# Performance work log

Measured on AMD Instinct MI355X. Metric: run time of the kernel, lower is better.

The kernel has to match this reference:

```python
import jax, jax.numpy as jnp
import numpy as np


def setup_inputs() -> dict:
    key = jax.random.key(0)
    k1, k2 = jax.random.split(key)
    B, N, D = 32, 2048, 3
    x = jax.random.normal(k1, (B, N, D), dtype=jnp.float32)
    y = jax.random.normal(k2, (B, N, D), dtype=jnp.float32)
    return {"x": x, "y": y}


def reference(x, y):
    # Batched squared euclidean distance matrix [B, N, M] without
    # materializing the [B, N, M, D] difference tensor.
    x2 = jnp.sum(x * x, axis=-1)                      # [B, N]
    y2 = jnp.sum(y * y, axis=-1)                      # [B, M]
    xy = jnp.einsum('bnd,bmd->bnm', x, y)             # [B, N, M]
    dist = x2[:, :, None] + y2[:, None, :] - 2.0 * xy # squared cdist
    dist = jnp.maximum(dist, 0.0)
    in_dist_out = jnp.min(dist, axis=1)               # min over N -> [B, M]
    out_dist_in = jnp.min(dist, axis=2)               # min over M -> [B, N]
    num_pts = x.shape[0]                              # batch size, per original
    loss = jnp.sum(in_dist_out + out_dist_in) / num_pts
    return loss
```

## Files before the change

### kernel.cpp

```cpp
#include <hip/hip_runtime.h>


typedef __attribute__((ext_vector_type(8)))  short bf16x8;
typedef __attribute__((ext_vector_type(16))) float f32x16;
typedef __attribute__((ext_vector_type(4)))  unsigned int u32x4;

constexpr int B_SZ    = 32;
constexpr int NPTS    = 2048;
constexpr int BLOCK   = 256;
constexpr int STRIPES = 8;
constexpr int RT      = 2;
constexpr int CT      = NPTS / 32;
constexpr int CSTRIDE = 33;

__device__ __forceinline__ unsigned short f2bf(float f) {
    unsigned int u = __float_as_uint(f);
    u += 0x7FFFu + ((u >> 16) & 1u);
    return (unsigned short)(u >> 16);
}
__device__ __forceinline__ float bf2f(unsigned short h) {
    return __uint_as_float(((unsigned int)h) << 16);
}
__device__ __forceinline__ unsigned int pk(unsigned short lo, unsigned short hi) {
    return (unsigned int)lo | ((unsigned int)hi << 16);
}

__global__ __launch_bounds__(BLOCK, 2)
void chamfer_fused(const float* __restrict__ x, const float* __restrict__ y,
                   float* __restrict__ out) {
    __shared__ u32x4 blds[CT * 64];
    __shared__ float wsum[BLOCK / 64];

    const int bid    = blockIdx.x;
    const int stripe = bid & (STRIPES - 1);
    const int b      = (bid >> 3) & 31;
    const int dir    = bid >> 8;

    const float* q = ((dir == 0) ? x : y) + (size_t)b * NPTS * 3;
    const float* p = ((dir == 0) ? y : x) + (size_t)b * NPTS * 3;

    for (int pi = threadIdx.x; pi < NPTS; pi += BLOCK) {
        const float vx = p[pi * 3 + 0], vy = p[pi * 3 + 1], vz = p[pi * 3 + 2];
        const unsigned short hx = f2bf(vx), hy = f2bf(vy), hz = f2bf(vz);
        const unsigned short lx = f2bf(vx - bf2f(hx));
        const unsigned short ly = f2bf(vy - bf2f(hy));
        const unsigned short lz = f2bf(vz - bf2f(hz));
        const float h = 0.5f * fmaf(vx, vx, fmaf(vy, vy, vz * vz));
        const unsigned short hh = f2bf(h);
        const unsigned short hl = f2bf(h - bf2f(hh));
        const int ct = pi >> 5, col = pi & 31;
        u32x4 g0 = {pk(hx, hy), pk(hz, lx), pk(ly, lz), pk(hx, hy)};
        u32x4 g1 = {pk(hz, hh), pk(hl, 0), 0u, 0u};
        blds[ct * 64 + col]      = g0;
        blds[ct * 64 + 32 + col] = g1;
    }

    const int w    = threadIdx.x >> 6;
    const int lane = threadIdx.x & 63;
    const int g    = lane >> 5;
    const int r32  = lane & 31;
    bf16x8 afrag[RT];
    #pragma unroll
    for (int rt = 0; rt < RT; ++rt) {
        const int row = stripe * 256 + w * (RT * 32) + rt * 32 + r32;
        const float vx = q[row * 3 + 0], vy = q[row * 3 + 1], vz = q[row * 3 + 2];
        const unsigned short hx = f2bf(vx) ^ 0x8000, hy = f2bf(vy) ^ 0x8000,
                             hz = f2bf(vz) ^ 0x8000;
        const unsigned short lx = f2bf(vx - bf2f(hx ^ 0x8000)) ^ 0x8000;
        const unsigned short ly = f2bf(vy - bf2f(hy ^ 0x8000)) ^ 0x8000;
        const unsigned short lz = f2bf(vz - bf2f(hz ^ 0x8000)) ^ 0x8000;
        u32x4 fr;
        if (g == 0)
            fr = (u32x4){pk(hx, hy), pk(hz, hx), pk(hy, hz), pk(lx, ly)};
        else
            fr = (u32x4){pk(lz, 0x3F80), pk(0x3F80, 0), 0u, 0u};
        afrag[rt] = __builtin_bit_cast(bf16x8, fr);
    }
    __syncthreads();

    const f32x16 z = {0.f,0.f,0.f,0.f,0.f,0.f,0.f,0.f,
                      0.f,0.f,0.f,0.f,0.f,0.f,0.f,0.f};
    f32x16 rmin[RT];
    #pragma unroll
    for (int rt = 0; rt < RT; ++rt)
        #pragma unroll
        for (int j = 0; j < 16; ++j) rmin[rt][j] = 3.0e38f;

    #pragma unroll 2
    for (int ct = 0; ct < CT; ct += 2) {
        const bf16x8 b0 = __builtin_bit_cast(bf16x8, blds[ct * 64 + lane]);
        const bf16x8 b1 = __builtin_bit_cast(bf16x8, blds[ct * 64 + 64 + lane]);
        #pragma unroll
        for (int rt = 0; rt < RT; ++rt) {
            f32x16 a0 = __builtin_amdgcn_mfma_f32_32x32x16_bf16(afrag[rt], b0, z, 0, 0, 0);
            f32x16 a1 = __builtin_amdgcn_mfma_f32_32x32x16_bf16(afrag[rt], b1, z, 0, 0, 0);
            #pragma unroll
            for (int j = 0; j < 16; ++j)
                rmin[rt][j] = fminf(fminf(a0[j], a1[j]), rmin[rt][j]);
        }
    }

    __syncthreads();
    float* colm = (float*)blds;
    #pragma unroll
    for (int rt = 0; rt < RT; ++rt)
        #pragma unroll
        for (int j = 0; j < 16; ++j) {
            const int row = w * (RT * 32) + rt * 32 + (j & 3) + 8 * (j >> 2) + 4 * g;
            colm[row * CSTRIDE + r32] = rmin[rt][j];
        }
    __syncthreads();

    const int t = threadIdx.x;
    float v[32];
    #pragma unroll
    for (int k = 0; k < 32; ++k) v[k] = colm[t * CSTRIDE + k];
    #pragma unroll
    for (int s = 16; s > 0; s >>= 1)
        #pragma unroll
        for (int i = 0; i < s; ++i) v[i] = fminf(v[i], v[i + s]);

    const int grow = stripe * 256 + t;
    const float qx = q[grow * 3 + 0], qy = q[grow * 3 + 1], qz = q[grow * 3 + 2];
    const float q2 = fmaf(qx, qx, fmaf(qy, qy, qz * qz));
    float s = fmaxf(0.0f, fmaf(2.0f, v[0], q2));
    #pragma unroll
    for (int off = 32; off > 0; off >>= 1) s += __shfl_down(s, off, 64);
    if ((t & 63) == 0) wsum[t >> 6] = s;
    __syncthreads();
    if (t == 0) {
        float tt = 0.f;
        #pragma unroll
        for (int wv = 0; wv < BLOCK / 64; ++wv) tt += wsum[wv];
        atomicAdd(out, tt * (1.0f / B_SZ));
    }
}

extern "C" void kernel_launch(void* const* d_in, const int* in_sizes, int n_in,
                              void* d_out, int out_size, void* d_ws, size_t ws_size,
                              hipStream_t stream) {
    const float* x = (const float*)d_in[0];
    const float* y = (const float*)d_in[1];
    float* out = (float*)d_out;

    hipMemsetAsync(out, 0, sizeof(float) * out_size, stream);
    chamfer_fused<<<2 * B_SZ * STRIPES, BLOCK, 0, stream>>>(x, y, out);
}
```

Baseline: 71.23 us.

## Use 512-thread blocks with one row tile per wave and setprio around MFMAs

Doubles the block size so each of eight waves owns a single 32-row tile instead of two, which halves per-wave MFMA work and register pressure and raises the occupancy target in launch bounds. It wraps the MFMA pair in s_setprio to favour matrix issue, and replaces the padded column-min staging with an XOR-style rotated layout so the LDS stride is exactly 32. The trade-off is that each B fragment loaded from LDS is now reused by only one row tile, so LDS read traffic per MFMA doubles, and half the threads sit idle during the final reduction.

```diff
diff --git a/kernel.cpp b/kernel.cpp
--- a/kernel.cpp
+++ b/kernel.cpp
@@ -7,11 +7,9 @@
 
 constexpr int B_SZ    = 32;
 constexpr int NPTS    = 2048;
-constexpr int BLOCK   = 256;
+constexpr int BLOCK   = 512;
 constexpr int STRIPES = 8;
-constexpr int RT      = 2;
 constexpr int CT      = NPTS / 32;
-constexpr int CSTRIDE = 33;
 
 __device__ __forceinline__ unsigned short f2bf(float f) {
     unsigned int u = __float_as_uint(f);
@@ -25,7 +23,7 @@
     return (unsigned int)lo | ((unsigned int)hi << 16);
 }
 
-__global__ __launch_bounds__(BLOCK, 2)
+__global__ __launch_bounds__(BLOCK, 4)
 void chamfer_fused(const float* __restrict__ x, const float* __restrict__ y,
                    float* __restrict__ out) {
     __shared__ u32x4 blds[CT * 64];
@@ -59,10 +57,9 @@
     const int lane = threadIdx.x & 63;
     const int g    = lane >> 5;
     const int r32  = lane & 31;
-    bf16x8 afrag[RT];
-    #pragma unroll
-    for (int rt = 0; rt < RT; ++rt) {
-        const int row = stripe * 256 + w * (RT * 32) + rt * 32 + r32;
+    const int row  = stripe * 256 + w * 32 + r32;
+    bf16x8 afrag;
+    {
         const float vx = q[row * 3 + 0], vy = q[row * 3 + 1], vz = q[row * 3 + 2];
         const unsigned short hx = f2bf(vx) ^ 0x8000, hy = f2bf(vy) ^ 0x8000,
                              hz = f2bf(vz) ^ 0x8000;
@@ -74,56 +71,54 @@
             fr = (u32x4){pk(hx, hy), pk(hz, hx), pk(hy, hz), pk(lx, ly)};
         else
             fr = (u32x4){pk(lz, 0x3F80), pk(0x3F80, 0), 0u, 0u};
-        afrag[rt] = __builtin_bit_cast(bf16x8, fr);
+        afrag = __builtin_bit_cast(bf16x8, fr);
     }
     __syncthreads();
 
     const f32x16 z = {0.f,0.f,0.f,0.f,0.f,0.f,0.f,0.f,
                       0.f,0.f,0.f,0.f,0.f,0.f,0.f,0.f};
-    f32x16 rmin[RT];
+    f32x16 rmin;
     #pragma unroll
-    for (int rt = 0; rt < RT; ++rt)
-        #pragma unroll
-        for (int j = 0; j < 16; ++j) rmin[rt][j] = 3.0e38f;
+    for (int j = 0; j < 16; ++j) rmin[j] = 3.0e38f;
 
     #pragma unroll 2
     for (int ct = 0; ct < CT; ct += 2) {
         const bf16x8 b0 = __builtin_bit_cast(bf16x8, blds[ct * 64 + lane]);
         const bf16x8 b1 = __builtin_bit_cast(bf16x8, blds[ct * 64 + 64 + lane]);
+        __builtin_amdgcn_s_setprio(1);
+        f32x16 a0 = __builtin_amdgcn_mfma_f32_32x32x16_bf16(afrag, b0, z, 0, 0, 0);
+        f32x16 a1 = __builtin_amdgcn_mfma_f32_32x32x16_bf16(afrag, b1, z, 0, 0, 0);
+        __builtin_amdgcn_s_setprio(0);
         #pragma unroll
-        for (int rt = 0; rt < RT; ++rt) {
-            f32x16 a0 = __builtin_amdgcn_mfma_f32_32x32x16_bf16(afrag[rt], b0, z, 0, 0, 0);
-            f32x16 a1 = __builtin_amdgcn_mfma_f32_32x32x16_bf16(afrag[rt], b1, z, 0, 0, 0);
-            #pragma unroll
-            for (int j = 0; j < 16; ++j)
-                rmin[rt][j] = fminf(fminf(a0[j], a1[j]), rmin[rt][j]);
-        }
+        for (int j = 0; j < 16; ++j)
+            rmin[j] = fminf(fminf(a0[j], a1[j]), rmin[j]);
     }
 
     __syncthreads();
     float* colm = (float*)blds;
     #pragma unroll
-    for (int rt = 0; rt < RT; ++rt)
-        #pragma unroll
-        for (int j = 0; j < 16; ++j) {
-            const int row = w * (RT * 32) + rt * 32 + (j & 3) + 8 * (j >> 2) + 4 * g;
-            colm[row * CSTRIDE + r32] = rmin[rt][j];
-        }
+    for (int j = 0; j < 16; ++j) {
+        const int lr = w * 32 + (j & 3) + 8 * (j >> 2) + 4 * g;
+        colm[lr * 32 + ((r32 + lr) & 31)] = rmin[j];
+    }
     __syncthreads();
 
     const int t = threadIdx.x;
-    float v[32];
-    #pragma unroll
-    for (int k = 0; k < 32; ++k) v[k] = colm[t * CSTRIDE + k];
-    #pragma unroll
-    for (int s = 16; s > 0; s >>= 1)
+    float s = 0.0f;
+    if (t < 256) {
+        float v[32];
         #pragma unroll
-        for (int i = 0; i < s; ++i) v[i] = fminf(v[i], v[i + s]);
+        for (int k = 0; k < 32; ++k) v[k] = colm[t * 32 + ((k + t) & 31)];
+        #pragma unroll
+        for (int st = 16; st > 0; st >>= 1)
+            #pragma unroll
+            for (int i = 0; i < st; ++i) v[i] = fminf(v[i], v[i + st]);
+        const int grow = stripe * 256 + t;
+        const float qx = q[grow * 3 + 0], qy = q[grow * 3 + 1], qz = q[grow * 3 + 2];
+        const float q2 = fmaf(qx, qx, fmaf(qy, qy, qz * qz));
+        s = fmaxf(0.0f, fmaf(2.0f, v[0], q2));
+    }
 
-    const int grow = stripe * 256 + t;
-    const float qx = q[grow * 3 + 0], qy = q[grow * 3 + 1], qz = q[grow * 3 + 2];
-    const float q2 = fmaf(qx, qx, fmaf(qy, qy, qz * qz));
-    float s = fmaxf(0.0f, fmaf(2.0f, v[0], q2));
     #pragma unroll
     for (int off = 32; off > 0; off >>= 1) s += __shfl_down(s, off, 64);
     if ((t & 63) == 0) wsum[t >> 6] = s;
```

Result: no change. 70.04 us (-1.7%).

## Split candidate points across blocks with atomicMin workspace and separate reduce kernel

Applied to the files above, without the earlier changes.

Each block now processes only half of the candidate point set, doubling the grid, and writes per-query minima through atomicMin on the float bits into a workspace pre-filled with 0xFF. A second kernel sums the workspace and accumulates the loss. The column-min transpose uses a rotated (swizzled) LDS index instead of padding, and the launch bound asks for 3 blocks per CU. This halves LDS per block to raise occupancy and parallelism, at the cost of an extra memset, a second kernel launch and global atomics.

```diff
diff --git a/kernel.cpp b/kernel.cpp
--- a/kernel.cpp
+++ b/kernel.cpp
@@ -9,9 +9,11 @@
 constexpr int NPTS    = 2048;
 constexpr int BLOCK   = 256;
 constexpr int STRIPES = 8;
+constexpr int CSPLIT  = 2;
+constexpr int CPTS    = NPTS / CSPLIT;
+constexpr int CT      = CPTS / 32;
 constexpr int RT      = 2;
-constexpr int CT      = NPTS / 32;
-constexpr int CSTRIDE = 33;
+constexpr int NQ      = 2 * B_SZ * NPTS;
 
 __device__ __forceinline__ unsigned short f2bf(float f) {
     unsigned int u = __float_as_uint(f);
@@ -25,21 +27,21 @@
     return (unsigned int)lo | ((unsigned int)hi << 16);
 }
 
-__global__ __launch_bounds__(BLOCK, 2)
-void chamfer_fused(const float* __restrict__ x, const float* __restrict__ y,
-                   float* __restrict__ out) {
+__global__ __launch_bounds__(BLOCK, 3)
+void chamfer_main(const float* __restrict__ x, const float* __restrict__ y,
+                  unsigned int* __restrict__ ws) {
     __shared__ u32x4 blds[CT * 64];
-    __shared__ float wsum[BLOCK / 64];
 
     const int bid    = blockIdx.x;
-    const int stripe = bid & (STRIPES - 1);
-    const int b      = (bid >> 3) & 31;
-    const int dir    = bid >> 8;
+    const int ch     = bid & (CSPLIT - 1);
+    const int stripe = (bid >> 1) & (STRIPES - 1);
+    const int b      = (bid >> 4) & 31;
+    const int dir    = bid >> 9;
 
     const float* q = ((dir == 0) ? x : y) + (size_t)b * NPTS * 3;
-    const float* p = ((dir == 0) ? y : x) + (size_t)b * NPTS * 3;
+    const float* p = ((dir == 0) ? y : x) + (size_t)b * NPTS * 3 + ch * CPTS * 3;
 
-    for (int pi = threadIdx.x; pi < NPTS; pi += BLOCK) {
+    for (int pi = threadIdx.x; pi < CPTS; pi += BLOCK) {
         const float vx = p[pi * 3 + 0], vy = p[pi * 3 + 1], vz = p[pi * 3 + 2];
         const unsigned short hx = f2bf(vx), hy = f2bf(vy), hz = f2bf(vz);
         const unsigned short lx = f2bf(vx - bf2f(hx));
@@ -106,33 +108,40 @@
     for (int rt = 0; rt < RT; ++rt)
         #pragma unroll
         for (int j = 0; j < 16; ++j) {
-            const int row = w * (RT * 32) + rt * 32 + (j & 3) + 8 * (j >> 2) + 4 * g;
-            colm[row * CSTRIDE + r32] = rmin[rt][j];
+            const int lr = w * (RT * 32) + rt * 32 + (j & 3) + 8 * (j >> 2) + 4 * g;
+            colm[lr * 32 + ((r32 + lr) & 31)] = rmin[rt][j];
         }
     __syncthreads();
 
     const int t = threadIdx.x;
     float v[32];
     #pragma unroll
-    for (int k = 0; k < 32; ++k) v[k] = colm[t * CSTRIDE + k];
+    for (int k = 0; k < 32; ++k) v[k] = colm[t * 32 + ((k + t) & 31)];
     #pragma unroll
-    for (int s = 16; s > 0; s >>= 1)
+    for (int st = 16; st > 0; st >>= 1)
         #pragma unroll
-        for (int i = 0; i < s; ++i) v[i] = fminf(v[i], v[i + s]);
+        for (int i = 0; i < st; ++i) v[i] = fminf(v[i], v[i + st]);
 
     const int grow = stripe * 256 + t;
     const float qx = q[grow * 3 + 0], qy = q[grow * 3 + 1], qz = q[grow * 3 + 2];
     const float q2 = fmaf(qx, qx, fmaf(qy, qy, qz * qz));
-    float s = fmaxf(0.0f, fmaf(2.0f, v[0], q2));
+    const float d2 = fmaxf(0.0f, fmaf(2.0f, v[0], q2));
+    atomicMin(ws + (size_t)(dir * B_SZ + b) * NPTS + grow, __float_as_uint(d2));
+}
+
+__global__ __launch_bounds__(256)
+void chamfer_reduce(const float* __restrict__ ws, float* __restrict__ out) {
+    __shared__ float wsum[4];
+    const int i = blockIdx.x * 256 + threadIdx.x;
+    float4 vv = ((const float4*)ws)[i];
+    float s = (vv.x + vv.y) + (vv.z + vv.w);
     #pragma unroll
     for (int off = 32; off > 0; off >>= 1) s += __shfl_down(s, off, 64);
-    if ((t & 63) == 0) wsum[t >> 6] = s;
+    if ((threadIdx.x & 63) == 0) wsum[threadIdx.x >> 6] = s;
     __syncthreads();
-    if (t == 0) {
-        float tt = 0.f;
-        #pragma unroll
-        for (int wv = 0; wv < BLOCK / 64; ++wv) tt += wsum[wv];
-        atomicAdd(out, tt * (1.0f / B_SZ));
+    if (threadIdx.x == 0) {
+        float t = (wsum[0] + wsum[1]) + (wsum[2] + wsum[3]);
+        atomicAdd(out, t * (1.0f / B_SZ));
     }
 }
 
@@ -142,7 +151,11 @@
     const float* x = (const float*)d_in[0];
     const float* y = (const float*)d_in[1];
     float* out = (float*)d_out;
+    unsigned int* ws = (unsigned int*)d_ws;
 
     hipMemsetAsync(out, 0, sizeof(float) * out_size, stream);
-    chamfer_fused<<<2 * B_SZ * STRIPES, BLOCK, 0, stream>>>(x, y, out);
+    hipMemsetAsync(ws, 0xFF, (size_t)NQ * sizeof(unsigned int), stream);
+
+    chamfer_main<<<2 * B_SZ * STRIPES * CSPLIT, BLOCK, 0, stream>>>(x, y, ws);
+    chamfer_reduce<<<NQ / 4 / 256, 256, 0, stream>>>((const float*)ws, out);
 }
```

After: 72.28 us. About the same (+1.5%).
